# Kernel optimization log

Hardware: AMD Instinct MI355X
Metric: run time of the kernel (lower is better)

Reference implementation:

```python
import jax, jax.numpy as jnp
import numpy as np

D = 1024      # in_features
H = 768       # hidden_features per routed expert
E = 8         # n_routed_experts
K = 2         # n_activated_experts
NS = 2        # n_shared_experts
ROUTE_SCALE = 1.0


def setup_inputs() -> dict:
    key = jax.random.key(0)
    ks = jax.random.split(key, 6)
    s = 0.02
    return {
        "x": jax.random.normal(ks[0], (2, 1024, D), jnp.float32),
        "gate_w": jax.random.normal(ks[1], (E, D), jnp.float32) * s,
        "W1": jax.random.normal(ks[2], (E, 2 * H, D), jnp.float32) * s,   # expert fc1 (y|gate)
        "W2": jax.random.normal(ks[3], (E, D, H), jnp.float32) * s,       # expert fc2
        "Ws1": jax.random.normal(ks[4], (2 * NS * H, D), jnp.float32) * s,  # shared fc1
        "Ws2": jax.random.normal(ks[5], (D, NS * H), jnp.float32) * s,      # shared fc2
    }


def _gated_mlp(x, w1, w2):
    # GatedMLP: fc1 -> chunk(2) -> y * silu(gate) -> fc2, all bias-free
    h = x @ w1.T
    y, g = jnp.split(h, 2, axis=-1)
    return (y * jax.nn.silu(g)) @ w2.T


def reference(x, gate_w, W1, W2, Ws1, Ws2):
    x_shape = x.shape
    xf = x.reshape(-1, D)                 # [T, D]
    T = xf.shape[0]

    # --- Gate: softmax scores in fp32, top-k routing ---
    scores = jax.nn.softmax((xf @ gate_w.T).astype(jnp.float32), axis=-1)  # [T, E]
    top_vals, top_idx = jax.lax.top_k(scores, K)
    # no bias branch (in_features != 7168): gathered original scores == top_k values
    weights = (top_vals * ROUTE_SCALE).astype(x.dtype)                      # [T, K]

    # Dense per-token/expert combine weights (0 for unselected experts);
    # mathematically identical to the per-expert gather/scatter-add combine.
    w_dense = jnp.zeros((T, E), x.dtype).at[jnp.arange(T)[:, None], top_idx].set(weights)

    # --- Routed experts (stacked GatedMLPs) ---
    h = jnp.einsum('td,ehd->teh', xf, W1)        # [T, E, 2H]
    y, g = jnp.split(h, 2, axis=-1)
    eo = jnp.einsum('teh,edh->ted', y * jax.nn.silu(g), W2)  # [T, E, D]
    z = jnp.einsum('te,ted->td', w_dense, eo)    # weighted combine

    # --- Shared experts ---
    z = z + _gated_mlp(xf, Ws1, Ws2)
    return z.reshape(x_shape)
```

## Files before the change

### kernel.cpp

```cpp
#include <hip/hip_runtime.h>
#include <hip/hip_bf16.h>


typedef short bf16x8 __attribute__((ext_vector_type(8)));
typedef float f32x4 __attribute__((ext_vector_type(4)));

__device__ __forceinline__ unsigned short f2b(float f) {
    __hip_bfloat16 h = __float2bfloat16(f);
    return *reinterpret_cast<unsigned short*>(&h);
}

__device__ __forceinline__ void ldst16(const unsigned short* g, unsigned short* l) {
    __builtin_amdgcn_global_load_lds(
        (const __attribute__((address_space(1))) unsigned int*)g,
        (__attribute__((address_space(3))) unsigned int*)l, 16, 0, 0);
}

__device__ __forceinline__ void cvt8(const float* s, unsigned short* d, int j) {
    const float4* sp = reinterpret_cast<const float4*>(s) + (size_t)j * 2;
    float4 v0 = sp[0], v1 = sp[1];
    union { unsigned short u[8]; uint4 v; } o;
    o.u[0]=f2b(v0.x); o.u[1]=f2b(v0.y); o.u[2]=f2b(v0.z); o.u[3]=f2b(v0.w);
    o.u[4]=f2b(v1.x); o.u[5]=f2b(v1.y); o.u[6]=f2b(v1.z); o.u[7]=f2b(v1.w);
    *(reinterpret_cast<uint4*>(d) + j) = o.v;
}

__global__ __launch_bounds__(256) void k_convgate(const float* __restrict__ x,
                                                  const float* __restrict__ gw,
                                                  const float* __restrict__ W1,
                                                  const float* __restrict__ Ws1,
                                                  const float* __restrict__ W2,
                                                  const float* __restrict__ Ws2,
                                                  unsigned short* __restrict__ xb,
                                                  unsigned short* __restrict__ W1b,
                                                  unsigned short* __restrict__ Ws1b,
                                                  unsigned short* __restrict__ W2b,
                                                  unsigned short* __restrict__ Ws2b,
                                                  int* __restrict__ tokslot,
                                                  float* __restrict__ wroute,
                                                  int* __restrict__ cnt,
                                                  float* __restrict__ out) {
    __shared__ float red[4][8];
    __shared__ float sc[8];
    const int b = blockIdx.x, tid = threadIdx.x;
    if (b < 2880) {
        for (int q = 0; q < 4; q++) {
            int i = b * 1024 + q * 256 + tid;
            if (i < 1572864)       cvt8(W1,  W1b,  i);
            else if (i < 1966080)  cvt8(Ws1, Ws1b, i - 1572864);
            else if (i < 2752512)  cvt8(W2,  W2b,  i - 1966080);
            else                   cvt8(Ws2, Ws2b, i - 2752512);
        }
        return;
    }
    const int t = b - 2880;
    const int lane = tid & 63, w = tid >> 6;

    float4 v = reinterpret_cast<const float4*>(x + (size_t)t * 1024)[tid];
    union { unsigned short u[4]; } o;
    o.u[0]=f2b(v.x); o.u[1]=f2b(v.y); o.u[2]=f2b(v.z); o.u[3]=f2b(v.w);
    reinterpret_cast<ushort4*>(xb + (size_t)t * 1024)[tid] = *(ushort4*)o.u;

    float p[8];
    for (int e = 0; e < 8; e++) {
        float4 g = reinterpret_cast<const float4*>(gw + (size_t)e * 1024)[tid];
        p[e] = v.x*g.x + v.y*g.y + v.z*g.z + v.w*g.w;
    }
    for (int e = 0; e < 8; e++)
        for (int off = 32; off > 0; off >>= 1) p[e] += __shfl_down(p[e], off, 64);
    if (lane == 0)
        for (int e = 0; e < 8; e++) red[w][e] = p[e];
    __syncthreads();
    if (tid < 8) sc[tid] = red[0][tid] + red[1][tid] + red[2][tid] + red[3][tid];
    __syncthreads();
    if (tid == 0) {
        float m = sc[0];
        for (int e = 1; e < 8; e++) m = fmaxf(m, sc[e]);
        float ex[8], sum = 0.f;
        for (int e = 0; e < 8; e++) { ex[e] = expf(sc[e] - m); sum += ex[e]; }
        float inv = 1.f / sum;
        int i1 = 0;
        for (int e = 1; e < 8; e++) if (sc[e] > sc[i1]) i1 = e;
        int i2 = -1; float s2 = -1e30f;
        for (int e = 0; e < 8; e++) if (e != i1 && sc[e] > s2) { s2 = sc[e]; i2 = e; }
        int p1 = atomicAdd(&cnt[i1 * 16], 1);
        tokslot[i1 * 2048 + p1] = t; wroute[i1 * 2048 + p1] = ex[i1] * inv;
        int p2 = atomicAdd(&cnt[i2 * 16], 1);
        tokslot[i2 * 2048 + p2] = t; wroute[i2 * 2048 + p2] = ex[i2] * inv;
    }
    reinterpret_cast<float4*>(out + (size_t)t * 1024)[tid] = (float4){0.f, 0.f, 0.f, 0.f};
}

__global__ __launch_bounds__(256) void k_fc1u(const unsigned short* __restrict__ xb,
                                              const unsigned short* __restrict__ W1b,
                                              const unsigned short* __restrict__ Ws1b,
                                              const int* __restrict__ tokslot,
                                              const float* __restrict__ wroute,
                                              const int* __restrict__ cnt,
                                              unsigned short* __restrict__ act_r,
                                              unsigned short* __restrict__ acts) {
    __shared__ alignas(16) unsigned short As[128 * 32];
    __shared__ alignas(16) unsigned short Bs[128 * 32];
    const int tid = threadIdx.x, lane = tid & 63, w = tid >> 6;
    const int wr = w >> 1, wc = w & 1;
    const int mt = blockIdx.x / 12, ht = blockIdx.x % 12;
    const int h0 = ht * 64;

    int pre = 0, sel = -1, base = 0;
    for (int ee = 0; ee < 10; ee++) {
        int til = (ee < 8) ? ((cnt[ee * 16] + 127) >> 7) : 16;
        if (sel < 0 && mt < pre + til) { sel = ee; base = pre; }
        pre += til;
    }
    if (sel < 0) return;
    const int e = sel, m0 = (mt - base) * 128;
    const int Te = (e < 8) ? cnt[e * 16] : 2048;
    const unsigned short* Bp = (e < 8) ? (W1b + (size_t)e * 1536 * 1024)
                                       : (Ws1b + (size_t)(e - 8) * 768 * 1024);
    const int gOff = (e < 8) ? 768 : 1536;

    int aoff[2], boff[2];
    for (int q = 0; q < 2; q++) {
        int ch = q * 256 + tid;
        int row = ch >> 2, c = ch & 3;
        int ko = ((c ^ ((row >> 1) & 3)) << 3);
        int idx = m0 + row;
        int tk = (e < 8) ? ((idx < Te) ? tokslot[e * 2048 + idx] : 0) : idx;
        aoff[q] = tk * 1024 + ko;
        int grow = (row < 64) ? (h0 + row) : (gOff + h0 + row - 64);
        boff[q] = grow * 1024 + ko;
    }

    f32x4 accy[4][2], accg[4][2];
    for (int i = 0; i < 4; i++)
        for (int j = 0; j < 2; j++) {
            accy[i][j] = (f32x4){0.f, 0.f, 0.f, 0.f};
            accg[i][j] = (f32x4){0.f, 0.f, 0.f, 0.f};
        }

    const int cq = lane >> 4, lm = lane & 15;
    for (int k0 = 0; k0 < 1024; k0 += 32) {
        for (int q = 0; q < 2; q++) {
            ldst16(xb + aoff[q] + k0, As + (q * 256 + tid) * 8);
            ldst16(Bp + boff[q] + k0, Bs + (q * 256 + tid) * 8);
        }
        __syncthreads();
        bf16x8 a[4], by[2], bg[2];
        for (int i = 0; i < 4; i++) {
            int r = 64 * wr + 16 * i + lm;
            a[i] = *(const bf16x8*)&As[r * 32 + ((cq ^ ((r >> 1) & 3)) << 3)];
        }
        for (int j = 0; j < 2; j++) {
            int ry = 32 * wc + 16 * j + lm;
            by[j] = *(const bf16x8*)&Bs[ry * 32 + ((cq ^ ((ry >> 1) & 3)) << 3)];
            int rg = 64 + ry;
            bg[j] = *(const bf16x8*)&Bs[rg * 32 + ((cq ^ ((rg >> 1) & 3)) << 3)];
        }
        for (int i = 0; i < 4; i++)
            for (int j = 0; j < 2; j++) {
                accy[i][j] = __builtin_amdgcn_mfma_f32_16x16x32_bf16(a[i], by[j], accy[i][j], 0, 0, 0);
                accg[i][j] = __builtin_amdgcn_mfma_f32_16x16x32_bf16(a[i], bg[j], accg[i][j], 0, 0, 0);
            }
        __syncthreads();
    }

    for (int i = 0; i < 4; i++)
        for (int r2 = 0; r2 < 4; r2++) {
            int irow = m0 + 64 * wr + 16 * i + ((lane >> 4) << 2) + r2;
            if (irow >= Te) continue;
            float sw = (e < 8) ? wroute[e * 2048 + irow] : 1.0f;
            unsigned short* dst = (e < 8)
                ? (act_r + ((size_t)e * 2048 + irow) * 768)
                : (acts + (size_t)irow * 1536 + (size_t)(e - 8) * 768);
            for (int j = 0; j < 2; j++) {
                float y = accy[i][j][r2], g = accg[i][j][r2];
                float sg = g / (1.0f + __expf(-g));
                dst[h0 + 32 * wc + 16 * j + lm] = f2b(sw * y * sg);
            }
        }
}

__global__ __launch_bounds__(256) void k_fc2u(const unsigned short* __restrict__ act_r,
                                              const unsigned short* __restrict__ acts,
                                              const unsigned short* __restrict__ W2b,
                                              const unsigned short* __restrict__ Ws2b,
                                              const int* __restrict__ tokslot,
                                              const int* __restrict__ cnt,
                                              float* __restrict__ out) {
    __shared__ alignas(16) unsigned short As[128 * 64];
    __shared__ alignas(16) unsigned short Bs[64 * 64];
    const int tid = threadIdx.x, lane = tid & 63, w = tid >> 6;
    const int wr = w >> 1, wc = w & 1;
    const int mt = blockIdx.x >> 4, nt = blockIdx.x & 15;
    const int n0 = nt * 64;

    int e, m0, K, astride, bstride, Te;
    const unsigned short *Ab, *Bb;
    if (mt < 16) {
        e = 8; m0 = mt * 128; K = 1536; astride = 1536; bstride = 1536; Te = 2048;
        Ab = acts; Bb = Ws2b;
    } else {
        int rmt = mt - 16;
        int pre = 0, sel = -1, base = 0;
        for (int ee = 0; ee < 8; ee++) {
            int til = (cnt[ee * 16] + 127) >> 7;
            if (sel < 0 && rmt < pre + til) { sel = ee; base = pre; }
            pre += til;
        }
        if (sel < 0) return;
        e = sel; m0 = (rmt - base) * 128; K = 768; astride = 768; bstride = 768;
        Te = cnt[e * 16];
        Ab = act_r + (size_t)e * 2048 * 768;
        Bb = W2b + (size_t)e * 1024 * 768;
    }

    int aoff[4], boff[2];
    for (int q = 0; q < 4; q++) {
        int ch = q * 256 + tid;
        int row = ch >> 3, c = ch & 7;
        aoff[q] = (m0 + row) * astride + ((c ^ (row & 7)) << 3);
    }
    for (int q = 0; q < 2; q++) {
        int ch = q * 256 + tid;
        int row = ch >> 3, c = ch & 7;
        boff[q] = (n0 + row) * bstride + ((c ^ (row & 7)) << 3);
    }

    f32x4 acc[4][2];
    for (int i = 0; i < 4; i++)
        for (int j = 0; j < 2; j++) acc[i][j] = (f32x4){0.f, 0.f, 0.f, 0.f};

    const int lm = lane & 15;
    for (int k0 = 0; k0 < K; k0 += 64) {
        for (int q = 0; q < 4; q++) ldst16(Ab + aoff[q] + k0, As + (q * 256 + tid) * 8);
        for (int q = 0; q < 2; q++) ldst16(Bb + boff[q] + k0, Bs + (q * 256 + tid) * 8);
        __syncthreads();
        for (int kh = 0; kh < 2; kh++) {
            const int cq = kh * 4 + (lane >> 4);
            bf16x8 a[4], b[2];
            for (int i = 0; i < 4; i++) {
                int r = 64 * wr + 16 * i + lm;
                a[i] = *(const bf16x8*)&As[r * 64 + ((cq ^ (r & 7)) << 3)];
            }
            for (int j = 0; j < 2; j++) {
                int rb = 32 * wc + 16 * j + lm;
                b[j] = *(const bf16x8*)&Bs[rb * 64 + ((cq ^ (rb & 7)) << 3)];
            }
            for (int i = 0; i < 4; i++)
                for (int j = 0; j < 2; j++)
                    acc[i][j] = __builtin_amdgcn_mfma_f32_16x16x32_bf16(a[i], b[j], acc[i][j], 0, 0, 0);
        }
        __syncthreads();
    }

    for (int i = 0; i < 4; i++)
        for (int r2 = 0; r2 < 4; r2++) {
            int irow = m0 + 64 * wr + 16 * i + ((lane >> 4) << 2) + r2;
            if (irow >= Te) continue;
            int t = (e < 8) ? tokslot[e * 2048 + irow] : irow;
            for (int j = 0; j < 2; j++) {
                int col = n0 + 32 * wc + 16 * j + lm;
                atomicAdd(out + (size_t)t * 1024 + col, acc[i][j][r2]);
            }
        }
}

extern "C" void kernel_launch(void* const* d_in, const int* in_sizes, int n_in,
                              void* d_out, int out_size, void* d_ws, size_t ws_size,
                              hipStream_t stream) {
    const float* x   = (const float*)d_in[0];
    const float* gw  = (const float*)d_in[1];
    const float* W1  = (const float*)d_in[2];
    const float* W2  = (const float*)d_in[3];
    const float* Ws1 = (const float*)d_in[4];
    const float* Ws2 = (const float*)d_in[5];
    float* out = (float*)d_out;

    char* ws = (char*)d_ws;
    unsigned short* xb    = (unsigned short*)(ws + 0);
    unsigned short* W1b   = (unsigned short*)(ws + 4194304);
    unsigned short* Ws1b  = (unsigned short*)(ws + 29360128);
    unsigned short* W2b   = (unsigned short*)(ws + 35651584);
    unsigned short* Ws2b  = (unsigned short*)(ws + 48234496);
    unsigned short* act_r = (unsigned short*)(ws + 51380224);
    unsigned short* acts  = (unsigned short*)(ws + 76546048);
    int*            tokslot = (int*)(ws + 82837504);
    float*          wroute  = (float*)(ws + 82903040);
    int*            cnt     = (int*)(ws + 82968576);

    hipMemsetAsync(cnt, 0, 512, stream);
    k_convgate<<<4928, 256, 0, stream>>>(x, gw, W1, Ws1, W2, Ws2,
                                         xb, W1b, Ws1b, W2b, Ws2b,
                                         tokslot, wroute, cnt, out);
    k_fc1u<<<864, 256, 0, stream>>>(xb, W1b, Ws1b, tokslot, wroute, cnt, act_r, acts);
    k_fc2u<<<896, 256, 0, stream>>>(act_r, acts, W2b, Ws2b, tokslot, cnt, out);
}
```

Baseline: 237.6 us.

## Fuse MoE stages into one persistent kernel with grid barriers and atomic tile queue

Merges the conversion/gate, fc1 and fc2 kernels into a single persistent kernel of 448 blocks that uses spin-wait grid barriers between stages and atomic work counters to hand out tiles dynamically. The fc1 stage also moves from a 32-wide to a 64-wide K step per LDS load. The aim is to remove kernel launch gaps and tail effects between stages. In exchange it relies on all 448 blocks being co-resident, which could deadlock if occupancy is insufficient, and each stage now runs on fewer blocks.

```diff
diff --git a/kernel.cpp b/kernel.cpp
--- a/kernel.cpp
+++ b/kernel.cpp
@@ -4,6 +4,8 @@
 
 typedef short bf16x8 __attribute__((ext_vector_type(8)));
 typedef float f32x4 __attribute__((ext_vector_type(4)));
+
+#define NBLK 448
 
 __device__ __forceinline__ unsigned short f2b(float f) {
     __hip_bfloat16 h = __float2bfloat16(f);
@@ -25,244 +27,262 @@
     *(reinterpret_cast<uint4*>(d) + j) = o.v;
 }
 
-__global__ __launch_bounds__(256) void k_convgate(const float* __restrict__ x,
-                                                  const float* __restrict__ gw,
-                                                  const float* __restrict__ W1,
-                                                  const float* __restrict__ Ws1,
-                                                  const float* __restrict__ W2,
-                                                  const float* __restrict__ Ws2,
-                                                  unsigned short* __restrict__ xb,
-                                                  unsigned short* __restrict__ W1b,
-                                                  unsigned short* __restrict__ Ws1b,
-                                                  unsigned short* __restrict__ W2b,
-                                                  unsigned short* __restrict__ Ws2b,
-                                                  int* __restrict__ tokslot,
-                                                  float* __restrict__ wroute,
-                                                  int* __restrict__ cnt,
-                                                  float* __restrict__ out) {
+__device__ __forceinline__ void gbar(int* ctr) {
+    __syncthreads();
+    if (threadIdx.x == 0) {
+        __threadfence();
+        atomicAdd(ctr, 1);
+        while (__hip_atomic_load(ctr, __ATOMIC_ACQUIRE, __HIP_MEMORY_SCOPE_AGENT) < NBLK)
+            __builtin_amdgcn_s_sleep(2);
+        __threadfence();
+    }
+    __syncthreads();
+}
+
+__global__ __launch_bounds__(256, 2) void k_moe(const float* __restrict__ x,
+                                                const float* __restrict__ gw,
+                                                const float* __restrict__ W1,
+                                                const float* __restrict__ W2,
+                                                const float* __restrict__ Ws1,
+                                                const float* __restrict__ Ws2,
+                                                unsigned short* __restrict__ xb,
+                                                unsigned short* __restrict__ W1b,
+                                                unsigned short* __restrict__ Ws1b,
+                                                unsigned short* __restrict__ W2b,
+                                                unsigned short* __restrict__ Ws2b,
+                                                unsigned short* __restrict__ act_r,
+                                                unsigned short* __restrict__ acts,
+                                                int* __restrict__ tokslot,
+                                                float* __restrict__ wroute,
+                                                int* __restrict__ cnt,
+                                                int* __restrict__ ctl,
+                                                float* __restrict__ out) {
+    __shared__ alignas(16) unsigned short smem[16384];
     __shared__ float red[4][8];
     __shared__ float sc[8];
-    const int b = blockIdx.x, tid = threadIdx.x;
-    if (b < 2880) {
-        for (int q = 0; q < 4; q++) {
-            int i = b * 1024 + q * 256 + tid;
-            if (i < 1572864)       cvt8(W1,  W1b,  i);
-            else if (i < 1966080)  cvt8(Ws1, Ws1b, i - 1572864);
-            else if (i < 2752512)  cvt8(W2,  W2b,  i - 1966080);
-            else                   cvt8(Ws2, Ws2b, i - 2752512);
+    __shared__ int sTile;
+    const int tid = threadIdx.x, b = blockIdx.x;
+    const int lane = tid & 63, w = tid >> 6;
+
+    for (int i = b * 256 + tid; i < 3211264; i += NBLK * 256) {
+        if (i < 1572864)       cvt8(W1,  W1b,  i);
+        else if (i < 1966080)  cvt8(Ws1, Ws1b, i - 1572864);
+        else if (i < 2752512)  cvt8(W2,  W2b,  i - 1966080);
+        else if (i < 2949120)  cvt8(Ws2, Ws2b, i - 2752512);
+        else                   cvt8(x,   xb,   i - 2949120);
+    }
+    {
+        float4 z = (float4){0.f, 0.f, 0.f, 0.f};
+        float4* o4 = reinterpret_cast<float4*>(out);
+        for (int i = b * 256 + tid; i < 524288; i += NBLK * 256) o4[i] = z;
+    }
+    for (int t = b; t < 2048; t += NBLK) {
+        float4 v = reinterpret_cast<const float4*>(x + (size_t)t * 1024)[tid];
+        float p[8];
+        for (int e = 0; e < 8; e++) {
+            float4 g = reinterpret_cast<const float4*>(gw + (size_t)e * 1024)[tid];
+            p[e] = v.x*g.x + v.y*g.y + v.z*g.z + v.w*g.w;
         }
-        return;
-    }
-    const int t = b - 2880;
-    const int lane = tid & 63, w = tid >> 6;
-
-    float4 v = reinterpret_cast<const float4*>(x + (size_t)t * 1024)[tid];
-    union { unsigned short u[4]; } o;
-    o.u[0]=f2b(v.x); o.u[1]=f2b(v.y); o.u[2]=f2b(v.z); o.u[3]=f2b(v.w);
-    reinterpret_cast<ushort4*>(xb + (size_t)t * 1024)[tid] = *(ushort4*)o.u;
-
-    float p[8];
-    for (int e = 0; e < 8; e++) {
-        float4 g = reinterpret_cast<const float4*>(gw + (size_t)e * 1024)[tid];
-        p[e] = v.x*g.x + v.y*g.y + v.z*g.z + v.w*g.w;
-    }
-    for (int e = 0; e < 8; e++)
-        for (int off = 32; off > 0; off >>= 1) p[e] += __shfl_down(p[e], off, 64);
-    if (lane == 0)
-        for (int e = 0; e < 8; e++) red[w][e] = p[e];
-    __syncthreads();
-    if (tid < 8) sc[tid] = red[0][tid] + red[1][tid] + red[2][tid] + red[3][tid];
-    __syncthreads();
-    if (tid == 0) {
-        float m = sc[0];
-        for (int e = 1; e < 8; e++) m = fmaxf(m, sc[e]);
-        float ex[8], sum = 0.f;
-        for (int e = 0; e < 8; e++) { ex[e] = expf(sc[e] - m); sum += ex[e]; }
-        float inv = 1.f / sum;
-        int i1 = 0;
-        for (int e = 1; e < 8; e++) if (sc[e] > sc[i1]) i1 = e;
-        int i2 = -1; float s2 = -1e30f;
-        for (int e = 0; e < 8; e++) if (e != i1 && sc[e] > s2) { s2 = sc[e]; i2 = e; }
-        int p1 = atomicAdd(&cnt[i1 * 16], 1);
-        tokslot[i1 * 2048 + p1] = t; wroute[i1 * 2048 + p1] = ex[i1] * inv;
-        int p2 = atomicAdd(&cnt[i2 * 16], 1);
-        tokslot[i2 * 2048 + p2] = t; wroute[i2 * 2048 + p2] = ex[i2] * inv;
-    }
-    reinterpret_cast<float4*>(out + (size_t)t * 1024)[tid] = (float4){0.f, 0.f, 0.f, 0.f};
-}
-
-__global__ __launch_bounds__(256) void k_fc1u(const unsigned short* __restrict__ xb,
-                                              const unsigned short* __restrict__ W1b,
-                                              const unsigned short* __restrict__ Ws1b,
-                                              const int* __restrict__ tokslot,
-                                              const float* __restrict__ wroute,
-                                              const int* __restrict__ cnt,
-                                              unsigned short* __restrict__ act_r,
-                                              unsigned short* __restrict__ acts) {
-    __shared__ alignas(16) unsigned short As[128 * 32];
-    __shared__ alignas(16) unsigned short Bs[128 * 32];
-    const int tid = threadIdx.x, lane = tid & 63, w = tid >> 6;
-    const int wr = w >> 1, wc = w & 1;
-    const int mt = blockIdx.x / 12, ht = blockIdx.x % 12;
-    const int h0 = ht * 64;
-
-    int pre = 0, sel = -1, base = 0;
-    for (int ee = 0; ee < 10; ee++) {
-        int til = (ee < 8) ? ((cnt[ee * 16] + 127) >> 7) : 16;
-        if (sel < 0 && mt < pre + til) { sel = ee; base = pre; }
-        pre += til;
-    }
-    if (sel < 0) return;
-    const int e = sel, m0 = (mt - base) * 128;
-    const int Te = (e < 8) ? cnt[e * 16] : 2048;
-    const unsigned short* Bp = (e < 8) ? (W1b + (size_t)e * 1536 * 1024)
-                                       : (Ws1b + (size_t)(e - 8) * 768 * 1024);
-    const int gOff = (e < 8) ? 768 : 1536;
-
-    int aoff[2], boff[2];
-    for (int q = 0; q < 2; q++) {
-        int ch = q * 256 + tid;
-        int row = ch >> 2, c = ch & 3;
-        int ko = ((c ^ ((row >> 1) & 3)) << 3);
-        int idx = m0 + row;
-        int tk = (e < 8) ? ((idx < Te) ? tokslot[e * 2048 + idx] : 0) : idx;
-        aoff[q] = tk * 1024 + ko;
-        int grow = (row < 64) ? (h0 + row) : (gOff + h0 + row - 64);
-        boff[q] = grow * 1024 + ko;
-    }
-
-    f32x4 accy[4][2], accg[4][2];
-    for (int i = 0; i < 4; i++)
-        for (int j = 0; j < 2; j++) {
-            accy[i][j] = (f32x4){0.f, 0.f, 0.f, 0.f};
-            accg[i][j] = (f32x4){0.f, 0.f, 0.f, 0.f};
-        }
-
-    const int cq = lane >> 4, lm = lane & 15;
-    for (int k0 = 0; k0 < 1024; k0 += 32) {
-        for (int q = 0; q < 2; q++) {
-            ldst16(xb + aoff[q] + k0, As + (q * 256 + tid) * 8);
-            ldst16(Bp + boff[q] + k0, Bs + (q * 256 + tid) * 8);
+        for (int e = 0; e < 8; e++)
+            for (int off = 32; off > 0; off >>= 1) p[e] += __shfl_down(p[e], off, 64);
+        if (lane == 0)
+            for (int e = 0; e < 8; e++) red[w][e] = p[e];
+        __syncthreads();
+        if (tid < 8) sc[tid] = red[0][tid] + red[1][tid] + red[2][tid] + red[3][tid];
+        __syncthreads();
+        if (tid == 0) {
+            float m = sc[0];
+            for (int e = 1; e < 8; e++) m = fmaxf(m, sc[e]);
+            float ex[8], sum = 0.f;
+            for (int e = 0; e < 8; e++) { ex[e] = expf(sc[e] - m); sum += ex[e]; }
+            float inv = 1.f / sum;
+            int i1 = 0;
+            for (int e = 1; e < 8; e++) if (sc[e] > sc[i1]) i1 = e;
+            int i2 = -1; float s2 = -1e30f;
+            for (int e = 0; e < 8; e++) if (e != i1 && sc[e] > s2) { s2 = sc[e]; i2 = e; }
+            int p1 = atomicAdd(&cnt[i1 * 16], 1);
+            tokslot[i1 * 2048 + p1] = t; wroute[i1 * 2048 + p1] = ex[i1] * inv;
+            int p2 = atomicAdd(&cnt[i2 * 16], 1);
+            tokslot[i2 * 2048 + p2] = t; wroute[i2 * 2048 + p2] = ex[i2] * inv;
         }
         __syncthreads();
-        bf16x8 a[4], by[2], bg[2];
-        for (int i = 0; i < 4; i++) {
-            int r = 64 * wr + 16 * i + lm;
-            a[i] = *(const bf16x8*)&As[r * 32 + ((cq ^ ((r >> 1) & 3)) << 3)];
+    }
+    gbar(&ctl[0]);
+
+    {
+        unsigned short* As = smem;
+        unsigned short* Bs = smem + 8192;
+        const int wr = w >> 1, wc = w & 1;
+        const int cqb = lane >> 4, lm = lane & 15;
+        for (;;) {
+            __syncthreads();
+            if (tid == 0) sTile = atomicAdd(&ctl[2], 1);
+            __syncthreads();
+            const int tile = sTile;
+            if (tile >= 864) break;
+            const int mt = tile / 12, ht = tile % 12;
+            const int h0 = ht * 64;
+            int pre = 0, sel = -1, base = 0;
+            for (int ee = 0; ee < 10; ee++) {
+                int til = (ee < 8) ? ((cnt[ee * 16] + 127) >> 7) : 16;
+                if (sel < 0 && mt < pre + til) { sel = ee; base = pre; }
+                pre += til;
+            }
+            if (sel < 0) continue;
+            const int e = sel, m0 = (mt - base) * 128;
+            const int Te = (e < 8) ? cnt[e * 16] : 2048;
+            const unsigned short* Bp = (e < 8) ? (W1b + (size_t)e * 1536 * 1024)
+                                               : (Ws1b + (size_t)(e - 8) * 768 * 1024);
+            const int gOff = (e < 8) ? 768 : 1536;
+
+            const int kc = tid & 7;
+            int aoff[4], boff[4];
+            for (int q = 0; q < 4; q++) {
+                int row = q * 32 + (tid >> 3);
+                int ko = ((kc ^ (row & 7)) << 3);
+                int idx = m0 + row;
+                int tk = (e < 8) ? ((idx < Te) ? tokslot[e * 2048 + idx] : 0) : idx;
+                aoff[q] = tk * 1024 + ko;
+                int grow = (row < 64) ? (h0 + row) : (gOff + h0 + row - 64);
+                boff[q] = grow * 1024 + ko;
+            }
+
+            f32x4 accy[4][2], accg[4][2];
+            for (int i = 0; i < 4; i++)
+                for (int j = 0; j < 2; j++) {
+                    accy[i][j] = (f32x4){0.f, 0.f, 0.f, 0.f};
+                    accg[i][j] = (f32x4){0.f, 0.f, 0.f, 0.f};
+                }
+
+            for (int k0 = 0; k0 < 1024; k0 += 64) {
+                for (int q = 0; q < 4; q++) {
+                    ldst16(xb + aoff[q] + k0, As + (q * 256 + tid) * 8);
+                    ldst16(Bp + boff[q] + k0, Bs + (q * 256 + tid) * 8);
+                }
+                __syncthreads();
+                for (int kh = 0; kh < 2; kh++) {
+                    const int cq = kh * 4 + cqb;
+                    bf16x8 a[4], by[2], bg[2];
+                    for (int i = 0; i < 4; i++) {
+                        int r = 64 * wr + 16 * i + lm;
+                        a[i] = *(const bf16x8*)&As[r * 64 + ((cq ^ (r & 7)) << 3)];
+                    }
+                    for (int j = 0; j < 2; j++) {
+                        int ry = 32 * wc + 16 * j + lm;
+                        by[j] = *(const bf16x8*)&Bs[ry * 64 + ((cq ^ (ry & 7)) << 3)];
+                        int rg = 64 + ry;
+                        bg[j] = *(const bf16x8*)&Bs[rg * 64 + ((cq ^ (rg & 7)) << 3)];
+                    }
+                    for (int i = 0; i < 4; i++)
+                        for (int j = 0; j < 2; j++) {
+                            accy[i][j] = __builtin_amdgcn_mfma_f32_16x16x32_bf16(a[i], by[j], accy[i][j], 0, 0, 0);
+                            accg[i][j] = __builtin_amdgcn_mfma_f32_16x16x32_bf16(a[i], bg[j], accg[i][j], 0, 0, 0);
+                        }
+                }
+                __syncthreads();
+            }
+
+            for (int i = 0; i < 4; i++)
+                for (int r2 = 0; r2 < 4; r2++) {
+                    int irow = m0 + 64 * wr + 16 * i + ((lane >> 4) << 2) + r2;
+                    if (irow >= Te) continue;
+                    float sw = (e < 8) ? wroute[e * 2048 + irow] : 1.0f;
+                    unsigned short* dst = (e < 8)
+                        ? (act_r + ((size_t)e * 2048 + irow) * 768)
+                        : (acts + (size_t)irow * 1536 + (size_t)(e - 8) * 768);
+                    for (int j = 0; j < 2; j++) {
+                        float y = accy[i][j][r2], g = accg[i][j][r2];
+                        float sg = g / (1.0f + __expf(-g));
+                        dst[h0 + 32 * wc + 16 * j + lm] = f2b(sw * y * sg);
+                    }
+                }
         }
-        for (int j = 0; j < 2; j++) {
-            int ry = 32 * wc + 16 * j + lm;
-            by[j] = *(const bf16x8*)&Bs[ry * 32 + ((cq ^ ((ry >> 1) & 3)) << 3)];
-            int rg = 64 + ry;
-            bg[j] = *(const bf16x8*)&Bs[rg * 32 + ((cq ^ ((rg >> 1) & 3)) << 3)];
+    }
+    gbar(&ctl[1]);
+
+    {
+        unsigned short* As = smem;
+        unsigned short* Bs = smem + 8192;
+        const int wr = w >> 1, wc = w & 1;
+        const int lm = lane & 15;
+        for (;;) {
+            __syncthreads();
+            if (tid == 0) sTile = atomicAdd(&ctl[3], 1);
+            __syncthreads();
+            const int tile = sTile;
+            if (tile >= 896) break;
+            const int mt = tile >> 4, nt = tile & 15;
+            const int n0 = nt * 64;
+            int e, m0, K, astride, bstride, Te;
+            const unsigned short *Ab, *Bb;
+            if (mt < 16) {
+                e = 8; m0 = mt * 128; K = 1536; astride = 1536; bstride = 1536; Te = 2048;
+                Ab = acts; Bb = Ws2b;
+            } else {
+                int rmt = mt - 16;
+                int pre = 0, sel = -1, base = 0;
+                for (int ee = 0; ee < 8; ee++) {
+                    int til = (cnt[ee * 16] + 127) >> 7;
+                    if (sel < 0 && rmt < pre + til) { sel = ee; base = pre; }
+                    pre += til;
+                }
+                if (sel < 0) continue;
+                e = sel; m0 = (rmt - base) * 128; K = 768; astride = 768; bstride = 768;
+                Te = cnt[e * 16];
+                Ab = act_r + (size_t)e * 2048 * 768;
+                Bb = W2b + (size_t)e * 1024 * 768;
+            }
+
+            int aoff[4], boff[2];
+            for (int q = 0; q < 4; q++) {
+                int ch = q * 256 + tid;
+                int row = ch >> 3, c = ch & 7;
+                aoff[q] = (m0 + row) * astride + ((c ^ (row & 7)) << 3);
+            }
+            for (int q = 0; q < 2; q++) {
+                int ch = q * 256 + tid;
+                int row = ch >> 3, c = ch & 7;
+                boff[q] = (n0 + row) * bstride + ((c ^ (row & 7)) << 3);
+            }
+
+            f32x4 acc[4][2];
+            for (int i = 0; i < 4; i++)
+                for (int j = 0; j < 2; j++) acc[i][j] = (f32x4){0.f, 0.f, 0.f, 0.f};
+
+            for (int k0 = 0; k0 < K; k0 += 64) {
+                for (int q = 0; q < 4; q++) ldst16(Ab + aoff[q] + k0, As + (q * 256 + tid) * 8);
+                for (int q = 0; q < 2; q++) ldst16(Bb + boff[q] + k0, Bs + (q * 256 + tid) * 8);
+                __syncthreads();
+                for (int kh = 0; kh < 2; kh++) {
+                    const int cq = kh * 4 + (lane >> 4);
+                    bf16x8 a[4], bb[2];
+                    for (int i = 0; i < 4; i++) {
+                        int r = 64 * wr + 16 * i + lm;
+                        a[i] = *(const bf16x8*)&As[r * 64 + ((cq ^ (r & 7)) << 3)];
+                    }
+                    for (int j = 0; j < 2; j++) {
+                        int rb = 32 * wc + 16 * j + lm;
+                        bb[j] = *(const bf16x8*)&Bs[rb * 64 + ((cq ^ (rb & 7)) << 3)];
+                    }
+                    for (int i = 0; i < 4; i++)
+                        for (int j = 0; j < 2; j++)
+                            acc[i][j] = __builtin_amdgcn_mfma_f32_16x16x32_bf16(a[i], bb[j], acc[i][j], 0, 0, 0);
+                }
+                __syncthreads();
+            }
+
+            for (int i = 0; i < 4; i++)
+                for (int r2 = 0; r2 < 4; r2++) {
+                    int irow = m0 + 64 * wr + 16 * i + ((lane >> 4) << 2) + r2;
+                    if (irow >= Te) continue;
+                    int t = (e < 8) ? tokslot[e * 2048 + irow] : irow;
+                    for (int j = 0; j < 2; j++) {
+                        int col = n0 + 32 * wc + 16 * j + lm;
+                        atomicAdd(out + (size_t)t * 1024 + col, acc[i][j][r2]);
+                    }
+                }
         }
-        for (int i = 0; i < 4; i++)
-            for (int j = 0; j < 2; j++) {
-                accy[i][j] = __builtin_amdgcn_mfma_f32_16x16x32_bf16(a[i], by[j], accy[i][j], 0, 0, 0);
-                accg[i][j] = __builtin_amdgcn_mfma_f32_16x16x32_bf16(a[i], bg[j], accg[i][j], 0, 0, 0);
-            }
-        __syncthreads();
-    }
-
-    for (int i = 0; i < 4; i++)
-        for (int r2 = 0; r2 < 4; r2++) {
-            int irow = m0 + 64 * wr + 16 * i + ((lane >> 4) << 2) + r2;
-            if (irow >= Te) continue;
-            float sw = (e < 8) ? wroute[e * 2048 + irow] : 1.0f;
-            unsigned short* dst = (e < 8)
-                ? (act_r + ((size_t)e * 2048 + irow) * 768)
-                : (acts + (size_t)irow * 1536 + (size_t)(e - 8) * 768);
-            for (int j = 0; j < 2; j++) {
-                float y = accy[i][j][r2], g = accg[i][j][r2];
-                float sg = g / (1.0f + __expf(-g));
-                dst[h0 + 32 * wc + 16 * j + lm] = f2b(sw * y * sg);
-            }
-        }
-}
-
-__global__ __launch_bounds__(256) void k_fc2u(const unsigned short* __restrict__ act_r,
-                                              const unsigned short* __restrict__ acts,
-                                              const unsigned short* __restrict__ W2b,
-                                              const unsigned short* __restrict__ Ws2b,
-                                              const int* __restrict__ tokslot,
-                                              const int* __restrict__ cnt,
-                                              float* __restrict__ out) {
-    __shared__ alignas(16) unsigned short As[128 * 64];
-    __shared__ alignas(16) unsigned short Bs[64 * 64];
-    const int tid = threadIdx.x, lane = tid & 63, w = tid >> 6;
-    const int wr = w >> 1, wc = w & 1;
-    const int mt = blockIdx.x >> 4, nt = blockIdx.x & 15;
-    const int n0 = nt * 64;
-
-    int e, m0, K, astride, bstride, Te;
-    const unsigned short *Ab, *Bb;
-    if (mt < 16) {
-        e = 8; m0 = mt * 128; K = 1536; astride = 1536; bstride = 1536; Te = 2048;
-        Ab = acts; Bb = Ws2b;
-    } else {
-        int rmt = mt - 16;
-        int pre = 0, sel = -1, base = 0;
-        for (int ee = 0; ee < 8; ee++) {
-            int til = (cnt[ee * 16] + 127) >> 7;
-            if (sel < 0 && rmt < pre + til) { sel = ee; base = pre; }
-            pre += til;
-        }
-        if (sel < 0) return;
-        e = sel; m0 = (rmt - base) * 128; K = 768; astride = 768; bstride = 768;
-        Te = cnt[e * 16];
-        Ab = act_r + (size_t)e * 2048 * 768;
-        Bb = W2b + (size_t)e * 1024 * 768;
-    }
-
-    int aoff[4], boff[2];
-    for (int q = 0; q < 4; q++) {
-        int ch = q * 256 + tid;
-        int row = ch >> 3, c = ch & 7;
-        aoff[q] = (m0 + row) * astride + ((c ^ (row & 7)) << 3);
-    }
-    for (int q = 0; q < 2; q++) {
-        int ch = q * 256 + tid;
-        int row = ch >> 3, c = ch & 7;
-        boff[q] = (n0 + row) * bstride + ((c ^ (row & 7)) << 3);
-    }
-
-    f32x4 acc[4][2];
-    for (int i = 0; i < 4; i++)
-        for (int j = 0; j < 2; j++) acc[i][j] = (f32x4){0.f, 0.f, 0.f, 0.f};
-
-    const int lm = lane & 15;
-    for (int k0 = 0; k0 < K; k0 += 64) {
-        for (int q = 0; q < 4; q++) ldst16(Ab + aoff[q] + k0, As + (q * 256 + tid) * 8);
-        for (int q = 0; q < 2; q++) ldst16(Bb + boff[q] + k0, Bs + (q * 256 + tid) * 8);
-        __syncthreads();
-        for (int kh = 0; kh < 2; kh++) {
-            const int cq = kh * 4 + (lane >> 4);
-            bf16x8 a[4], b[2];
-            for (int i = 0; i < 4; i++) {
-                int r = 64 * wr + 16 * i + lm;
-                a[i] = *(const bf16x8*)&As[r * 64 + ((cq ^ (r & 7)) << 3)];
-            }
-            for (int j = 0; j < 2; j++) {
-                int rb = 32 * wc + 16 * j + lm;
-                b[j] = *(const bf16x8*)&Bs[rb * 64 + ((cq ^ (rb & 7)) << 3)];
-            }
-            for (int i = 0; i < 4; i++)
-                for (int j = 0; j < 2; j++)
-                    acc[i][j] = __builtin_amdgcn_mfma_f32_16x16x32_bf16(a[i], b[j], acc[i][j], 0, 0, 0);
-        }
-        __syncthreads();
-    }
-
-    for (int i = 0; i < 4; i++)
-        for (int r2 = 0; r2 < 4; r2++) {
-            int irow = m0 + 64 * wr + 16 * i + ((lane >> 4) << 2) + r2;
-            if (irow >= Te) continue;
-            int t = (e < 8) ? tokslot[e * 2048 + irow] : irow;
-            for (int j = 0; j < 2; j++) {
-                int col = n0 + 32 * wc + 16 * j + lm;
-                atomicAdd(out + (size_t)t * 1024 + col, acc[i][j][r2]);
-            }
-        }
+    }
 }
 
 extern "C" void kernel_launch(void* const* d_in, const int* in_sizes, int n_in,
@@ -287,11 +307,10 @@
     int*            tokslot = (int*)(ws + 82837504);
     float*          wroute  = (float*)(ws + 82903040);
     int*            cnt     = (int*)(ws + 82968576);
-
-    hipMemsetAsync(cnt, 0, 512, stream);
-    k_convgate<<<4928, 256, 0, stream>>>(x, gw, W1, Ws1, W2, Ws2,
-                                         xb, W1b, Ws1b, W2b, Ws2b,
-                                         tokslot, wroute, cnt, out);
-    k_fc1u<<<864, 256, 0, stream>>>(xb, W1b, Ws1b, tokslot, wroute, cnt, act_r, acts);
-    k_fc2u<<<896, 256, 0, stream>>>(act_r, acts, W2b, Ws2b, tokslot, cnt, out);
-}
+    int*            ctl     = (int*)(ws + 82969088);
+
+    hipMemsetAsync(cnt, 0, 1024, stream);
+    k_moe<<<NBLK, 256, 0, stream>>>(x, gw, W1, W2, Ws1, Ws2,
+                                    xb, W1b, Ws1b, W2b, Ws2b,
+                                    act_r, acts, tokslot, wroute, cnt, ctl, out);
+}
```

Result: slower. 424.5 us (+78.6%).
